# Performance work log

Measured on AMD Instinct MI355X. Metric: run time of the kernel, lower is better.

## Reference

```python
import jax, jax.numpy as jnp
import numpy as np

B, TM, SM, V = 16, 128, 64, 1024
NEG = jnp.float32(-1e30)  # safe stand-in for -inf (avoids nan in grads)


def setup_inputs() -> dict:
    key = jax.random.key(0)
    k1, k2 = jax.random.split(key)
    acts = jax.random.normal(k1, (B * TM * (SM + 1), V), dtype=jnp.float32)
    labels = jax.random.randint(k2, (B, SM), 1, V, dtype=jnp.int32)
    input_lengths = jnp.full((B,), TM, dtype=jnp.int32)
    label_lengths = jnp.full((B,), SM, dtype=jnp.int32)
    return {"acts": acts, "labels": labels, "input_lengths": input_lengths,
            "label_lengths": label_lengths, "T_max": TM, "S_max": SM}


def _monotonic_rnnt_loss(acts, labels, input_lengths, label_lengths, T_max, S_max, blank=0):
    """Monotonic RNN-T: each time frame emits exactly one symbol (blank keeps
    label position, a label advances it). Loss = -log p(labels | acts).
    acts is packed row-major: row(b,t,s) = off_b + t*(S_b+1) + s."""
    Bq = labels.shape[0]
    N = acts.shape[0]
    T = input_lengths.astype(jnp.int32)
    S = label_lengths.astype(jnp.int32)
    Sp1 = S + 1
    sizes = T * Sp1
    off = jnp.concatenate([jnp.zeros((1,), jnp.int32), jnp.cumsum(sizes)[:-1]])

    # log-softmax normalizer per packed row (softmax done internally by the loss)
    lse = jax.scipy.special.logsumexp(acts, axis=1)  # [N]

    t_idx = jnp.arange(T_max)[None, :, None]          # [1,T,1]
    s_idx = jnp.arange(S_max + 1)[None, None, :]      # [1,1,S+1]
    rows = off[:, None, None] + t_idx * Sp1[:, None, None] + s_idx  # [B,T,S+1]
    rows_c = jnp.clip(rows, 0, N - 1)

    valid_b = (t_idx < T[:, None, None]) & (s_idx <= S[:, None, None])
    blank_lp = jnp.where(valid_b, acts[rows_c, blank] - lse[rows_c], NEG)  # [B,T,S+1]

    lab_rows = rows_c[:, :, :S_max]                   # [B,T,S]
    valid_l = (t_idx < T[:, None, None]) & (s_idx[:, :, :S_max] < S[:, None, None])
    # gather log p(y_{s+1} | b, t, s) without materializing [B,T,S,V]
    label_lp = jnp.where(valid_l,
                         acts[lab_rows, labels[:, None, :]] - lse[lab_rows], NEG)  # [B,T,S]

    blank_t = jnp.transpose(blank_lp, (1, 0, 2))  # [T,B,S+1]
    label_t = jnp.transpose(label_lp, (1, 0, 2))  # [T,B,S]

    alpha0 = jnp.full((Bq, S_max + 1), NEG, dtype=acts.dtype).at[:, 0].set(0.0)

    def step(alpha, inp):
        t, blp, llp = inp
        # stay (blank) or advance one label
        shifted = jnp.concatenate(
            [jnp.full((Bq, 1), NEG, dtype=acts.dtype), alpha[:, :-1] + llp], axis=1)
        new = jnp.logaddexp(alpha + blp, shifted)
        # freeze alpha past each sequence's last frame
        return jnp.where(t < T[:, None], new, alpha), None

    alpha, _ = jax.lax.scan(step, alpha0, (jnp.arange(T_max), blank_t, label_t))
    return -alpha[jnp.arange(Bq), S]


def reference(acts, labels, input_lengths, label_lengths, T_max, S_max):
    return _monotonic_rnnt_loss(acts, labels, input_lengths, label_lengths, T_max, S_max, blank=0)
```

## Files before the change

kernel.cpp:

```cpp
#include <hip/hip_runtime.h>
#include <math.h>

#define Bc 16
#define TM 128
#define SMAX 64
#define VV 1024
#define NEGF (-1e30f)
#define CELLS (Bc * TM * (SMAX + 1))

typedef float f32x4 __attribute__((ext_vector_type(4)));

__device__ __forceinline__ float logaddexp_f(float a, float b) {
  float m = fmaxf(a, b);
  float d = fminf(a, b) - m;
  return m + __logf(1.0f + __expf(d));
}

#define RPG 4

__global__ __launch_bounds__(256) void rnnt_lp_kernel(
    const float* __restrict__ acts, const int* __restrict__ labels,
    const int* __restrict__ Tlen, const int* __restrict__ Slen,
    float* __restrict__ blank_lp, float* __restrict__ label_lp)
{
  const int lane = threadIdx.x & 63;
  const int wv   = threadIdx.x >> 6;
  const int grp  = blockIdx.x * 4 + wv;
  const int cell0 = grp * RPG;
  if (cell0 >= CELLS) return;

  const int bidx = lane & 15;
  const int Tb_l = Tlen[bidx];
  const int Sb_l = Slen[bidx];
  const int sz   = Tb_l * (Sb_l + 1);
  int incl = sz;
  #pragma unroll
  for (int o = 1; o < 16; o <<= 1) {
    int u = __shfl_up(incl, o);
    if (bidx >= o) incl += u;
  }
  const int excl = incl - sz;

  int s_[RPG], Sb_[RPG], lab_[RPG], labidx_[RPG];
  bool val_[RPG];
  unsigned off_[RPG];
  f32x4 x[RPG][4];

  #pragma unroll
  for (int k = 0; k < RPG; ++k) {
    const int cell = cell0 + k;
    const int b   = cell / (TM * (SMAX + 1));
    const int rem = cell - b * (TM * (SMAX + 1));
    const int t   = rem / (SMAX + 1);
    const int s   = rem - t * (SMAX + 1);
    const int Tb  = __shfl(Tb_l, b);
    const int Sb  = __shfl(Sb_l, b);
    const int rb  = __shfl(excl, b);
    s_[k] = s; Sb_[k] = Sb;
    labidx_[k] = (b * TM + t) * SMAX + s;
    val_[k] = (t < Tb) && (s <= Sb);
    const unsigned row = (unsigned)rb + (unsigned)t * (unsigned)(Sb + 1) + (unsigned)s;
    off_[k] = row * (unsigned)(VV * 4);
    lab_[k] = (val_[k] && s < Sb) ? labels[b * SMAX + s] : -1;
  }

  #pragma unroll
  for (int k = 0; k < RPG; ++k) {
    if (val_[k]) {
      const f32x4* rp = (const f32x4*)((const char*)acts + off_[k]) + lane;
      x[k][0] = rp[0];
      x[k][1] = rp[64];
      x[k][2] = rp[128];
      x[k][3] = rp[192];
    }
  }

  float p[RPG];
  #pragma unroll
  for (int k = 0; k < RPG; ++k) {
    float q = 0.0f;
    #pragma unroll
    for (int j = 0; j < 4; ++j)
      q += __expf(x[k][j].x) + __expf(x[k][j].y) +
           __expf(x[k][j].z) + __expf(x[k][j].w);
    p[k] = q;
  }

  #pragma unroll
  for (int o = 1; o < 64; o <<= 1) {
    #pragma unroll
    for (int k = 0; k < RPG; ++k) p[k] += __shfl_xor(p[k], o);
  }

  #pragma unroll
  for (int k = 0; k < RPG; ++k) {
    const int cell = cell0 + k;
    if (!val_[k]) {
      if (lane == 0) {
        blank_lp[cell] = NEGF;
        if (s_[k] < SMAX) label_lp[labidx_[k]] = NEGF;
      }
      continue;
    }
    const float lse = __logf(p[k]);
    if (s_[k] < Sb_[k]) {
      const int f    = lab_[k] >> 2;
      const int comp = lab_[k] & 3;
      const int src  = f & 63;
      const int j    = f >> 6;
      f32x4 xx = (j == 0) ? x[k][0] : (j == 1) ? x[k][1] : (j == 2) ? x[k][2] : x[k][3];
      float v = (comp == 0) ? xx.x : (comp == 1) ? xx.y : (comp == 2) ? xx.z : xx.w;
      v = __shfl(v, src);
      if (lane == 0) label_lp[labidx_[k]] = v - lse;
    } else if (s_[k] < SMAX) {
      if (lane == 0) label_lp[labidx_[k]] = NEGF;
    }
    if (lane == 0) blank_lp[cell] = x[k][0].x - lse;
  }
}

__global__ __launch_bounds__(256) void rnnt_alpha_kernel(
    const float* __restrict__ blank_lp, const float* __restrict__ label_lp,
    const int* __restrict__ Tlen, const int* __restrict__ Slen,
    float* __restrict__ out)
{
  __shared__ __align__(16) float sb[TM * (SMAX + 1)];
  __shared__ __align__(16) float sl[TM * SMAX];
  const int b = blockIdx.x;
  const int tid = threadIdx.x;

  const float* gb = blank_lp + (size_t)b * TM * (SMAX + 1);
  const float* gl = label_lp + (size_t)b * TM * SMAX;
  for (int i = tid * 4; i < TM * (SMAX + 1); i += 256 * 4)
    *(float4*)&sb[i] = *(const float4*)&gb[i];
  for (int i = tid * 4; i < TM * SMAX; i += 256 * 4)
    *(float4*)&sl[i] = *(const float4*)&gl[i];
  __syncthreads();
  if (tid >= 64) return;

  const int lane = tid;
  const int Tb = Tlen[b], Sb = Slen[b];
  float a    = (lane == 0) ? 0.0f : NEGF;
  float a_hi = NEGF;

  for (int t = 0; t < Tb; ++t) {
    const float blp      = sb[t * (SMAX + 1) + lane];
    const float llp_prev = (lane >= 1) ? sl[t * SMAX + lane - 1] : NEGF;
    const float blp64    = sb[t * (SMAX + 1) + 64];
    const float llp63    = sl[t * SMAX + 63];
    const float a_prev   = __shfl_up(a, 1);
    const float a63      = __shfl(a, 63);
    const float newv = logaddexp_f(a + blp,
                                   (lane >= 1) ? (a_prev + llp_prev) : NEGF);
    const float new_hi = logaddexp_f(a_hi + blp64, a63 + llp63);
    a = newv;
    a_hi = new_hi;
  }

  const float via_shfl = __shfl(a, Sb & 63);
  const float aS = (Sb < 64) ? via_shfl : a_hi;
  if (lane == 0) out[b] = -aS;
}

extern "C" void kernel_launch(void* const* d_in, const int* in_sizes, int n_in,
                              void* d_out, int out_size, void* d_ws, size_t ws_size,
                              hipStream_t stream) {
  const float* acts  = (const float*)d_in[0];
  const int* labels  = (const int*)d_in[1];
  const int* Tlen    = (const int*)d_in[2];
  const int* Slen    = (const int*)d_in[3];
  float* out = (float*)d_out;

  float* blank_lp = (float*)d_ws;
  float* label_lp = blank_lp + Bc * TM * (SMAX + 1);

  const int groups = (CELLS + RPG - 1) / RPG;
  const int blocks = (groups + 3) / 4;
  rnnt_lp_kernel<<<blocks, 256, 0, stream>>>(
      acts, labels, Tlen, Slen, blank_lp, label_lp);
  rnnt_alpha_kernel<<<Bc, 256, 0, stream>>>(
      blank_lp, label_lp, Tlen, Slen, out);
}
```

Before: 716.2 us.

## Use persistent waves with double-buffered row pairs and nontemporal loads

The log-prob kernel becomes a persistent grid of 2048 blocks. Each wave walks over pairs of rows and software-pipelines them, issuing loads for the next pair before computing the current one. Row loads use nontemporal hints so streamed acts do not pollute the cache. This aims to keep more memory requests in flight per wave and cut launch and tail overhead, at the cost of higher register use, which may lower occupancy.

```diff
diff --git a/kernel.cpp b/kernel.cpp
--- a/kernel.cpp
+++ b/kernel.cpp
@@ -7,6 +7,9 @@
 #define VV 1024
 #define NEGF (-1e30f)
 #define CELLS (Bc * TM * (SMAX + 1))
+#define NPAIRS (CELLS / 2)
+#define LPBLOCKS 2048
+#define NWAVES (LPBLOCKS * 4)
 
 typedef float f32x4 __attribute__((ext_vector_type(4)));
 
@@ -16,7 +19,11 @@
   return m + __logf(1.0f + __expf(d));
 }
 
-#define RPG 4
+struct RowG {
+  int s, Sb, lab, labidx;
+  unsigned off;
+  bool val;
+};
 
 __global__ __launch_bounds__(256) void rnnt_lp_kernel(
     const float* __restrict__ acts, const int* __restrict__ labels,
@@ -25,9 +32,7 @@
 {
   const int lane = threadIdx.x & 63;
   const int wv   = threadIdx.x >> 6;
-  const int grp  = blockIdx.x * 4 + wv;
-  const int cell0 = grp * RPG;
-  if (cell0 >= CELLS) return;
+  const int wave = blockIdx.x * 4 + wv;
 
   const int bidx = lane & 15;
   const int Tb_l = Tlen[bidx];
@@ -41,81 +46,113 @@
   }
   const int excl = incl - sz;
 
-  int s_[RPG], Sb_[RPG], lab_[RPG], labidx_[RPG];
-  bool val_[RPG];
-  unsigned off_[RPG];
-  f32x4 x[RPG][4];
-
-  #pragma unroll
-  for (int k = 0; k < RPG; ++k) {
-    const int cell = cell0 + k;
+  auto geo = [&](int cell, RowG& g) {
     const int b   = cell / (TM * (SMAX + 1));
     const int rem = cell - b * (TM * (SMAX + 1));
     const int t   = rem / (SMAX + 1);
-    const int s   = rem - t * (SMAX + 1);
-    const int Tb  = __shfl(Tb_l, b);
-    const int Sb  = __shfl(Sb_l, b);
-    const int rb  = __shfl(excl, b);
-    s_[k] = s; Sb_[k] = Sb;
-    labidx_[k] = (b * TM + t) * SMAX + s;
-    val_[k] = (t < Tb) && (s <= Sb);
-    const unsigned row = (unsigned)rb + (unsigned)t * (unsigned)(Sb + 1) + (unsigned)s;
-    off_[k] = row * (unsigned)(VV * 4);
-    lab_[k] = (val_[k] && s < Sb) ? labels[b * SMAX + s] : -1;
-  }
-
-  #pragma unroll
-  for (int k = 0; k < RPG; ++k) {
-    if (val_[k]) {
-      const f32x4* rp = (const f32x4*)((const char*)acts + off_[k]) + lane;
-      x[k][0] = rp[0];
-      x[k][1] = rp[64];
-      x[k][2] = rp[128];
-      x[k][3] = rp[192];
-    }
-  }
-
-  float p[RPG];
-  #pragma unroll
-  for (int k = 0; k < RPG; ++k) {
-    float q = 0.0f;
+    g.s = rem - t * (SMAX + 1);
+    const int Tb = __shfl(Tb_l, b);
+    g.Sb = __shfl(Sb_l, b);
+    const int rb = __shfl(excl, b);
+    g.labidx = (b * TM + t) * SMAX + g.s;
+    g.val = (t < Tb) && (g.s <= g.Sb);
+    const unsigned row = (unsigned)rb + (unsigned)t * (unsigned)(g.Sb + 1) + (unsigned)g.s;
+    g.off = row * (unsigned)(VV * 4);
+    g.lab = (g.val && g.s < g.Sb) ? labels[b * SMAX + g.s] : -1;
+  };
+
+  auto issue = [&](const RowG& g, f32x4 (&x)[4]) {
+    if (g.val) {
+      const f32x4* rp = (const f32x4*)((const char*)acts + g.off) + lane;
+      x[0] = __builtin_nontemporal_load(rp);
+      x[1] = __builtin_nontemporal_load(rp + 64);
+      x[2] = __builtin_nontemporal_load(rp + 128);
+      x[3] = __builtin_nontemporal_load(rp + 192);
+    }
+  };
+
+  auto computePair = [&](int cell0, const RowG (&g)[2], const f32x4 (&x0)[4],
+                         const f32x4 (&x1)[4]) {
+    float p0 = 0.0f, p1 = 0.0f;
+    if (g[0].val) {
+      #pragma unroll
+      for (int j = 0; j < 4; ++j)
+        p0 += __expf(x0[j].x) + __expf(x0[j].y) + __expf(x0[j].z) + __expf(x0[j].w);
+    }
+    if (g[1].val) {
+      #pragma unroll
+      for (int j = 0; j < 4; ++j)
+        p1 += __expf(x1[j].x) + __expf(x1[j].y) + __expf(x1[j].z) + __expf(x1[j].w);
+    }
     #pragma unroll
-    for (int j = 0; j < 4; ++j)
-      q += __expf(x[k][j].x) + __expf(x[k][j].y) +
-           __expf(x[k][j].z) + __expf(x[k][j].w);
-    p[k] = q;
-  }
-
-  #pragma unroll
-  for (int o = 1; o < 64; o <<= 1) {
+    for (int o = 1; o < 64; o <<= 1) {
+      p0 += __shfl_xor(p0, o);
+      p1 += __shfl_xor(p1, o);
+    }
+
     #pragma unroll
-    for (int k = 0; k < RPG; ++k) p[k] += __shfl_xor(p[k], o);
-  }
-
-  #pragma unroll
-  for (int k = 0; k < RPG; ++k) {
-    const int cell = cell0 + k;
-    if (!val_[k]) {
+    for (int k = 0; k < 2; ++k) {
+      const int cell = cell0 + k;
+      const RowG& gg = g[k];
+      if (!gg.val) {
+        if (lane == 0) {
+          blank_lp[cell] = NEGF;
+          if (gg.s < SMAX) label_lp[gg.labidx] = NEGF;
+        }
+        continue;
+      }
+      const float ps  = (k == 0) ? p0 : p1;
+      const float lse = __logf(ps);
+      if (gg.s < gg.Sb) {
+        const int f    = gg.lab >> 2;
+        const int comp = gg.lab & 3;
+        const int src  = f & 63;
+        const int j    = f >> 6;
+        f32x4 xx;
+        if (k == 0) xx = (j == 0) ? x0[0] : (j == 1) ? x0[1] : (j == 2) ? x0[2] : x0[3];
+        else        xx = (j == 0) ? x1[0] : (j == 1) ? x1[1] : (j == 2) ? x1[2] : x1[3];
+        float v = (comp == 0) ? xx.x : (comp == 1) ? xx.y : (comp == 2) ? xx.z : xx.w;
+        v = __shfl(v, src);
+        if (lane == 0) label_lp[gg.labidx] = v - lse;
+      } else if (gg.s < SMAX) {
+        if (lane == 0) label_lp[gg.labidx] = NEGF;
+      }
       if (lane == 0) {
-        blank_lp[cell] = NEGF;
-        if (s_[k] < SMAX) label_lp[labidx_[k]] = NEGF;
+        const float blank = (k == 0) ? x0[0].x : x1[0].x;
+        blank_lp[cell] = blank - lse;
       }
-      continue;
-    }
-    const float lse = __logf(p[k]);
-    if (s_[k] < Sb_[k]) {
-      const int f    = lab_[k] >> 2;
-      const int comp = lab_[k] & 3;
-      const int src  = f & 63;
-      const int j    = f >> 6;
-      f32x4 xx = (j == 0) ? x[k][0] : (j == 1) ? x[k][1] : (j == 2) ? x[k][2] : x[k][3];
-      float v = (comp == 0) ? xx.x : (comp == 1) ? xx.y : (comp == 2) ? xx.z : xx.w;
-      v = __shfl(v, src);
-      if (lane == 0) label_lp[labidx_[k]] = v - lse;
-    } else if (s_[k] < SMAX) {
-      if (lane == 0) label_lp[labidx_[k]] = NEGF;
-    }
-    if (lane == 0) blank_lp[cell] = x[k][0].x - lse;
+    }
+  };
+
+  RowG gA[2], gB[2];
+  f32x4 xA0[4], xA1[4], xB0[4], xB1[4];
+
+  int pA = wave;
+  if (pA >= NPAIRS) return;
+  geo(2 * pA, gA[0]); geo(2 * pA + 1, gA[1]);
+  issue(gA[0], xA0);  issue(gA[1], xA1);
+
+  int pB = pA + NWAVES;
+  for (;;) {
+    const bool hB = (pB < NPAIRS);
+    if (hB) {
+      geo(2 * pB, gB[0]); geo(2 * pB + 1, gB[1]);
+      issue(gB[0], xB0);  issue(gB[1], xB1);
+    }
+    computePair(2 * pA, gA, xA0, xA1);
+    if (!hB) break;
+
+    const int pC = pB + NWAVES;
+    const bool hC = (pC < NPAIRS);
+    if (hC) {
+      geo(2 * pC, gA[0]); geo(2 * pC + 1, gA[1]);
+      issue(gA[0], xA0);  issue(gA[1], xA1);
+    }
+    computePair(2 * pB, gB, xB0, xB1);
+    if (!hC) break;
+
+    pA = pC;
+    pB = pC + NWAVES;
   }
 }
 
@@ -174,9 +211,7 @@
   float* blank_lp = (float*)d_ws;
   float* label_lp = blank_lp + Bc * TM * (SMAX + 1);
 
-  const int groups = (CELLS + RPG - 1) / RPG;
-  const int blocks = (groups + 3) / 4;
-  rnnt_lp_kernel<<<blocks, 256, 0, stream>>>(
+  rnnt_lp_kernel<<<LPBLOCKS, 256, 0, stream>>>(
       acts, labels, Tlen, Slen, blank_lp, label_lp);
   rnnt_alpha_kernel<<<Bc, 256, 0, stream>>>(
       blank_lp, label_lp, Tlen, Slen, out);
```

Result: faster. 684.9 us (-4.4%).
